# Kernel tuning notes

Measured on AMD Instinct MI355X. Metric: run time of the kernel, lower is better.

The kernel has to match this reference:

```python
import jax, jax.numpy as jnp
import numpy as np

N_QUBITS = 12
N_LAYERS = 2
DIM = 2 ** N_QUBITS  # 4096
BATCH = 1024


def _apply_gate(state, gate, qubit):
    """Apply a batched 2x2 gate to `qubit`. state: (b, 2^n) c64, gate: (b,2,2) c64.
    Mirrors torch _apply_single_qubit_gate: swap qubit axis to front, bmm, swap back."""
    b = state.shape[0]
    s = state.reshape((b,) + (2,) * N_QUBITS)
    ax = N_QUBITS - qubit  # qubit 0 is the last (least-significant) axis
    s = jnp.swapaxes(s, 1, ax)
    s = s.reshape(b, 2, DIM // 2)
    s = jnp.einsum('bij,bjk->bik', gate, s)
    s = s.reshape((b, 2) + (2,) * (N_QUBITS - 1))
    s = jnp.swapaxes(s, 1, ax)
    return s.reshape(b, DIM)


def _ry_gate(angle):
    """RY(theta) = [[cos(t/2), -sin(t/2)], [sin(t/2), cos(t/2)]]; angle: (b,)."""
    c = jnp.cos(angle / 2)
    s = jnp.sin(angle / 2)
    g = jnp.stack([jnp.stack([c, -s], axis=-1),
                   jnp.stack([s, c], axis=-1)], axis=-2)
    return g.astype(jnp.complex64)


def _apply_cnot(state, control, target):
    """CNOT: flip target amplitudes on the control=1 subspace."""
    b = state.shape[0]
    s = state.reshape((b,) + (2,) * N_QUBITS)
    ca = N_QUBITS - control
    ta = N_QUBITS - target
    s = jnp.moveaxis(s, (ca, ta), (1, 2))
    # control=0 slice unchanged; control=1 slice: swap target 0<->1 (flip)
    s = jnp.concatenate([s[:, :1], jnp.flip(s[:, 1:2], axis=2)], axis=1)
    s = jnp.moveaxis(s, (1, 2), (ca, ta))
    return s.reshape(b, DIM)


def _make_signs():
    # Pauli-Z expectation per qubit = sum_s probs[s] * (1 - 2*bit_q(s)); qubit 0 = LSB
    idx = np.arange(DIM)
    bits = (idx[:, None] >> np.arange(N_QUBITS)[None, :]) & 1
    return jnp.asarray(1.0 - 2.0 * bits, dtype=jnp.float32)  # (DIM, n_qubits)

SIGNS = _make_signs()


def setup_inputs() -> dict:
    key = jax.random.key(0)
    kx, kt = jax.random.split(key)
    x = jax.random.normal(kx, (BATCH, N_QUBITS), dtype=jnp.float32)
    thetas = 0.1 * jax.random.normal(kt, (N_LAYERS, N_QUBITS), dtype=jnp.float32)
    return {"x": x, "thetas": thetas}


def reference(x, thetas):
    b = x.shape[0]
    # |0>^n initial state
    state = jnp.zeros((b, DIM), dtype=jnp.complex64).at[:, 0].set(1.0)
    # angle encoding: RY(x_q) on each qubit
    for q in range(N_QUBITS):
        state = _apply_gate(state, _ry_gate(x[:, q]), q)
    # variational layers: RY(theta) per qubit, then cyclic CNOT ring
    for layer in range(N_LAYERS):
        for q in range(N_QUBITS):
            ang = jnp.broadcast_to(thetas[layer, q], (b,))
            state = _apply_gate(state, _ry_gate(ang), q)
        for q in range(N_QUBITS):
            state = _apply_cnot(state, q, (q + 1) % N_QUBITS)
    # Pauli-Z expectations on all qubits: (b, n_qubits)
    probs = jnp.abs(state) ** 2
    return probs @ SIGNS
```

## Files before the change

kernel.cpp:

```cpp
#include <hip/hip_runtime.h>

#define NQ    12
#define BATCH 1024

typedef float v2 __attribute__((ext_vector_type(2)));
typedef float v4 __attribute__((ext_vector_type(4)));

template<int P>
__device__ __forceinline__ void ryp_t(v2 A[16], float t) {
#pragma unroll
    for (int m = 0; m < 16; ++m) {
        if ((m & (1 << P)) == 0) {
            const int j = m | (1 << P);
            const v2 Ai = A[m], Aj = A[j];
            A[m] = Ai - t * Aj;
            A[j] = Aj + t * Ai;
        }
    }
}

__device__ __forceinline__ void ry0_t(v2 A[16], float t) {
    const v2 tv = v2{-t, t};
#pragma unroll
    for (int m = 0; m < 16; ++m) {
        const v2 sw = v2{A[m].y, A[m].x};
        A[m] = A[m] + tv * sw;
    }
}

__device__ __forceinline__ float rdlane(float v, int lane) {
    return __uint_as_float(__builtin_amdgcn_readlane(__float_as_uint(v), lane));
}

__global__ __launch_bounds__(128, 2)
void qc_kernel(const float* __restrict__ x, const float* __restrict__ th,
               float* __restrict__ out) {
    __shared__ __attribute__((aligned(16))) float buf1[2 * 32 * 68];
    __shared__ float obuf[12 * 2];

    const int b = blockIdx.x;
    const int w = threadIdx.x >> 6;
    const int l = threadIdx.x & 63;
    const float* xb = x + b * NQ;

    const int q_ = l & 31;
    float ang;
    if (l & 32) ang = (q_ < 12) ? 0.5f * th[NQ + q_] : 0.0f;
    else        { const int m_ = (q_ < 12) ? q_ : 11; ang = 0.5f * (xb[m_] + th[m_]); }
    float sv_, cv_;
    __sincosf(ang, &sv_, &cv_);
    const float tl = __fdividef(sv_, cv_);

    float pt = cv_;
    pt *= __shfl_xor(pt, 1, 64);
    pt *= __shfl_xor(pt, 2, 64);
    pt *= __shfl_xor(pt, 4, 64);
    pt *= __shfl_xor(pt, 8, 64);
    const float C = rdlane(pt, 32);

    float c_[NQ], s_[NQ], t1[NQ];
#pragma unroll
    for (int q = 0; q < NQ; ++q) {
        c_[q] = rdlane(cv_, q);
        s_[q] = rdlane(sv_, q);
        t1[q] = rdlane(tl, 32 + q);
    }

    const int l0=l&1, l1=(l>>1)&1, l2=(l>>2)&1, l3=(l>>3)&1, l4=(l>>4)&1, l5=(l>>5)&1;
    float GL = ((l1^l0) ? s_[6] : c_[6]) * ((l2^l1) ? s_[7] : c_[7]);
    GL *= ((l3^l2) ? s_[8] : c_[8]) * ((l4^l3) ? s_[9] : c_[9]);
    GL *= ((l5^l4) ? s_[10] : c_[10]) * ((w^l5) ? s_[11] : c_[11]);
    GL *= C;
    const float GL0 = GL * (l0 ? s_[5] : c_[5]);
    const float GL1 = GL * (l0 ? c_[5] : s_[5]);

    const float f0_0 = w ? s_[0] : c_[0], f0_1 = w ? c_[0] : s_[0];
    const float f1_0 = w ? s_[1] : c_[1], f1_1 = w ? c_[1] : s_[1];

    v2 A[16];
    A[0] = v2{f0_0 * f1_0, f0_1 * f1_1};
    A[1] = v2{f0_0 * f1_1, f0_1 * f1_0};
#pragma unroll
    for (int k = 2; k < 5; ++k) {
#pragma unroll
        for (int m = 0; m < (1 << (k - 1)); ++m) {
            const int bp = (m >> (k - 2)) & 1;
            A[m | (1 << (k - 1))] = A[m] * (bp ? c_[k] : s_[k]);
            A[m]                  = A[m] * (bp ? s_[k] : c_[k]);
        }
    }
#pragma unroll
    for (int m = 0; m < 16; ++m) A[m] *= (m & 8) ? GL1 : GL0;

    ry0_t(A, t1[0]);
    ryp_t<0>(A, t1[1]);
    ryp_t<1>(A, t1[2]);
    ryp_t<2>(A, t1[3]);
    ryp_t<3>(A, t1[4]);

    {
        float* wp = &buf1[w * 2176 + l];
#pragma unroll
        for (int m = 0; m < 16; ++m) {
            wp[(2*m)   * 68] = A[m].x;
            wp[(2*m+1) * 68] = A[m].y;
        }
    }
    __syncthreads();

    {
        const float s10 = (l & 32) ? t1[10] : -t1[10];
        const float s11 = w ? t1[11] : -t1[11];
        const int basec = (l & 31) * 68;
        const int ro = (l & 32);
        const int rf = ro ^ 32;
        const float* p00 = &buf1[ w      * 2176 + basec + ro];
        const float* p01 = &buf1[ w      * 2176 + basec + rf];
        const float* p10 = &buf1[(w ^ 1) * 2176 + basec + ro];
        const float* p11 = &buf1[(w ^ 1) * 2176 + basec + rf];
#pragma unroll
        for (int k = 0; k < 8; ++k) {
            const v4 a  = *reinterpret_cast<const v4*>(p00 + 4*k);
            const v4 bq = *reinterpret_cast<const v4*>(p01 + 4*k);
            const v4 cq = *reinterpret_cast<const v4*>(p10 + 4*k);
            const v4 dq = *reinterpret_cast<const v4*>(p11 + 4*k);
            const v4 u = a  + s10 * bq;
            const v4 v = cq + s10 * dq;
            const v4 r = u + s11 * v;
            A[2*k]   = v2{r.x, r.y};
            A[2*k+1] = v2{r.z, r.w};
        }
    }

    ry0_t(A, t1[5]);
    ryp_t<0>(A, t1[6]);
    ryp_t<1>(A, t1[7]);
    ryp_t<2>(A, t1[8]);
    ryp_t<3>(A, t1[9]);

#pragma unroll
    for (int m = 0; m < 16; ++m) A[m] *= A[m];

    float S = 0.f;
#pragma unroll
    for (int m = 0; m < 16; ++m) S += A[m].x + A[m].y;
    float d0[16];
#pragma unroll
    for (int m = 0; m < 16; ++m) d0[m] = A[m].x - A[m].y;
    float P1 = 0.f;
#pragma unroll
    for (int i = 0; i < 16; ++i) P1 += d0[i];
    float d1[8];
#pragma unroll
    for (int i = 0; i < 8; ++i) d1[i] = d0[2*i] - d0[2*i+1];
    float P3 = 0.f;
#pragma unroll
    for (int i = 0; i < 8; ++i) P3 += d1[i];
    float d2[4];
#pragma unroll
    for (int i = 0; i < 4; ++i) d2[i] = d1[2*i] - d1[2*i+1];
    const float P7  = d2[0] + d2[1] + d2[2] + d2[3];
    const float d3a = d2[0] - d2[1], d3b = d2[2] - d2[3];
    const float PF  = d3a + d3b;
    const float PV  = d3a - d3b;

    const int pl5 = __popc(l & 31) & 1;
    float y0 = pl5 ? -P1 : P1;
    float y1 = pl5 ? -P3 : P3;
    float y2 = pl5 ? -P7 : P7;
    float y3 = pl5 ? -PF : PF;
    y0 += __shfl_xor(y0, 1, 64); y1 += __shfl_xor(y1, 1, 64);
    y2 += __shfl_xor(y2, 1, 64); y3 += __shfl_xor(y3, 1, 64);
    y0 += __shfl_xor(y0, 2, 64); y1 += __shfl_xor(y1, 2, 64);
    y2 += __shfl_xor(y2, 2, 64); y3 += __shfl_xor(y3, 2, 64);
    const int g = l & 3;
    float y = (g == 0) ? y0 : (g == 1) ? y1 : (g == 2) ? y2 : y3;
    y += __shfl_xor(y,  4, 64);
    y += __shfl_xor(y,  8, 64);
    y += __shfl_xor(y, 16, 64);
    y += __shfl_xor(y, 32, 64);
    if (l < 4) obuf[(5 + l) * 2 + w] = y;

    float wS = S, wV = PV;
#pragma unroll
    for (int k = 0; k < 6; ++k) {
        float pS = __shfl_xor(wS, 1 << k, 64);
        wS = ((l >> k) & 1) ? (pS - wS) : (wS + pS);
        float pV = __shfl_xor(wV, 1 << k, 64);
        wV = ((l >> k) & 1) ? (pV - wV) : (wV + pV);
    }

    if (l == 3)  obuf[1*2 + w]  = wS;
    if (l == 7)  obuf[2*2 + w]  = wS;
    if (l == 15) obuf[3*2 + w]  = wS;
    if (l == 31) { obuf[4*2 + w] = wS; obuf[9*2 + w] = wV; }
    if (l == 62) obuf[0*2 + w]  = wV;
    if (l == 63) { obuf[10*2 + w] = wV; obuf[11*2 + w] = wV; }
    __syncthreads();

    if (threadIdx.x < NQ) {
        const int q = threadIdx.x;
        const float p0 = obuf[q*2 + 0], p1 = obuf[q*2 + 1];
        out[b * NQ + q] = (q == 0 || q == 11) ? (p0 - p1) : (p0 + p1);
    }
}

extern "C" void kernel_launch(void* const* d_in, const int* in_sizes, int n_in,
                              void* d_out, int out_size, void* d_ws, size_t ws_size,
                              hipStream_t stream) {
    const float* x  = (const float*)d_in[0];
    const float* th = (const float*)d_in[1];
    float* out = (float*)d_out;
    (void)in_sizes; (void)n_in; (void)out_size; (void)d_ws; (void)ws_size;

    qc_kernel<<<BATCH, 128, 0, stream>>>(x, th, out);
}
```

Before: 9.870 us.

## Pack four batch items per block and use DPP/swizzle for lane reductions

Each block now handles four batch elements with 512 threads instead of one element with 128, which cuts the grid to 256 blocks and gives each 128-thread group its own shared-memory slice. Cross-lane xor shuffles are replaced by DPP quad permutes and ds_swizzle, and the Walsh-style butterflies become FMA with a per-lane sign. The final parity reductions are also regrouped into vector adds. The bigger blocks use more shared memory each and share one __syncthreads, and with only 256 blocks on the device, occupancy and load balance may suffer.

```diff
diff --git a/kernel.cpp b/kernel.cpp
--- a/kernel.cpp
+++ b/kernel.cpp
@@ -32,16 +32,29 @@
     return __uint_as_float(__builtin_amdgcn_readlane(__float_as_uint(v), lane));
 }
 
-__global__ __launch_bounds__(128, 2)
+template<int CTRL>
+__device__ __forceinline__ float dppx(float v) {
+    return __int_as_float(__builtin_amdgcn_mov_dpp(__float_as_int(v), CTRL, 0xF, 0xF, true));
+}
+template<int PAT>
+__device__ __forceinline__ float swz(float v) {
+    return __int_as_float(__builtin_amdgcn_ds_swizzle(__float_as_int(v), PAT));
+}
+
+__global__ __launch_bounds__(512, 2)
 void qc_kernel(const float* __restrict__ x, const float* __restrict__ th,
                float* __restrict__ out) {
-    __shared__ __attribute__((aligned(16))) float buf1[2 * 32 * 68];
-    __shared__ float obuf[12 * 2];
-
-    const int b = blockIdx.x;
-    const int w = threadIdx.x >> 6;
-    const int l = threadIdx.x & 63;
+    __shared__ __attribute__((aligned(16))) float buf1[4 * 4352];
+    __shared__ float obuf[4 * 24];
+
+    const int tid = threadIdx.x;
+    const int p = tid >> 7;
+    const int w = (tid >> 6) & 1;
+    const int l = tid & 63;
+    const int b = blockIdx.x * 4 + p;
     const float* xb = x + b * NQ;
+    float* bufp  = &buf1[p * 4352];
+    float* obufp = &obuf[p * 24];
 
     const int q_ = l & 31;
     float ang;
@@ -52,10 +65,10 @@
     const float tl = __fdividef(sv_, cv_);
 
     float pt = cv_;
-    pt *= __shfl_xor(pt, 1, 64);
-    pt *= __shfl_xor(pt, 2, 64);
-    pt *= __shfl_xor(pt, 4, 64);
-    pt *= __shfl_xor(pt, 8, 64);
+    pt *= dppx<0xB1>(pt);
+    pt *= dppx<0x4E>(pt);
+    pt *= swz<0x101F>(pt);
+    pt *= swz<0x201F>(pt);
     const float C = rdlane(pt, 32);
 
     float c_[NQ], s_[NQ], t1[NQ];
@@ -99,7 +112,7 @@
     ryp_t<3>(A, t1[4]);
 
     {
-        float* wp = &buf1[w * 2176 + l];
+        float* wp = &bufp[w * 2176 + l];
 #pragma unroll
         for (int m = 0; m < 16; ++m) {
             wp[(2*m)   * 68] = A[m].x;
@@ -114,10 +127,10 @@
         const int basec = (l & 31) * 68;
         const int ro = (l & 32);
         const int rf = ro ^ 32;
-        const float* p00 = &buf1[ w      * 2176 + basec + ro];
-        const float* p01 = &buf1[ w      * 2176 + basec + rf];
-        const float* p10 = &buf1[(w ^ 1) * 2176 + basec + ro];
-        const float* p11 = &buf1[(w ^ 1) * 2176 + basec + rf];
+        const float* p00 = &bufp[ w      * 2176 + basec + ro];
+        const float* p01 = &bufp[ w      * 2176 + basec + rf];
+        const float* p10 = &bufp[(w ^ 1) * 2176 + basec + ro];
+        const float* p11 = &bufp[(w ^ 1) * 2176 + basec + rf];
 #pragma unroll
         for (int k = 0; k < 8; ++k) {
             const v4 a  = *reinterpret_cast<const v4*>(p00 + 4*k);
@@ -141,66 +154,68 @@
 #pragma unroll
     for (int m = 0; m < 16; ++m) A[m] *= A[m];
 
-    float S = 0.f;
-#pragma unroll
-    for (int m = 0; m < 16; ++m) S += A[m].x + A[m].y;
-    float d0[16];
-#pragma unroll
-    for (int m = 0; m < 16; ++m) d0[m] = A[m].x - A[m].y;
-    float P1 = 0.f;
-#pragma unroll
-    for (int i = 0; i < 16; ++i) P1 += d0[i];
-    float d1[8];
-#pragma unroll
-    for (int i = 0; i < 8; ++i) d1[i] = d0[2*i] - d0[2*i+1];
-    float P3 = 0.f;
-#pragma unroll
-    for (int i = 0; i < 8; ++i) P3 += d1[i];
-    float d2[4];
-#pragma unroll
-    for (int i = 0; i < 4; ++i) d2[i] = d1[2*i] - d1[2*i+1];
-    const float P7  = d2[0] + d2[1] + d2[2] + d2[3];
-    const float d3a = d2[0] - d2[1], d3b = d2[2] - d2[3];
-    const float PF  = d3a + d3b;
-    const float PV  = d3a - d3b;
+    v2 e[8], f[8];
+#pragma unroll
+    for (int i = 0; i < 8; ++i) { e[i] = A[2*i] + A[2*i+1]; f[i] = A[2*i] - A[2*i+1]; }
+    v2 se = ((e[0]+e[1]) + (e[2]+e[3])) + ((e[4]+e[5]) + (e[6]+e[7]));
+    v2 sf = ((f[0]+f[1]) + (f[2]+f[3])) + ((f[4]+f[5]) + (f[6]+f[7]));
+    v2 gq[4];
+#pragma unroll
+    for (int j = 0; j < 4; ++j) gq[j] = f[2*j] - f[2*j+1];
+    const v2 sg2 = (gq[0]+gq[1]) + (gq[2]+gq[3]);
+    const v2 h0 = gq[0] - gq[1], h1 = gq[2] - gq[3];
+    const v2 sh = h0 + h1;
+    const v2 iv = h0 - h1;
+    const float S  = se.x + se.y;
+    const float P1 = se.x - se.y;
+    const float P3 = sf.x - sf.y;
+    const float P7 = sg2.x - sg2.y;
+    const float PF = sh.x - sh.y;
+    const float PV = iv.x - iv.y;
 
     const int pl5 = __popc(l & 31) & 1;
     float y0 = pl5 ? -P1 : P1;
     float y1 = pl5 ? -P3 : P3;
     float y2 = pl5 ? -P7 : P7;
     float y3 = pl5 ? -PF : PF;
-    y0 += __shfl_xor(y0, 1, 64); y1 += __shfl_xor(y1, 1, 64);
-    y2 += __shfl_xor(y2, 1, 64); y3 += __shfl_xor(y3, 1, 64);
-    y0 += __shfl_xor(y0, 2, 64); y1 += __shfl_xor(y1, 2, 64);
-    y2 += __shfl_xor(y2, 2, 64); y3 += __shfl_xor(y3, 2, 64);
+    y0 += dppx<0xB1>(y0); y1 += dppx<0xB1>(y1);
+    y2 += dppx<0xB1>(y2); y3 += dppx<0xB1>(y3);
+    y0 += dppx<0x4E>(y0); y1 += dppx<0x4E>(y1);
+    y2 += dppx<0x4E>(y2); y3 += dppx<0x4E>(y3);
     const int g = l & 3;
     float y = (g == 0) ? y0 : (g == 1) ? y1 : (g == 2) ? y2 : y3;
-    y += __shfl_xor(y,  4, 64);
-    y += __shfl_xor(y,  8, 64);
-    y += __shfl_xor(y, 16, 64);
+    y += swz<0x101F>(y);
+    y += swz<0x201F>(y);
+    y += swz<0x401F>(y);
     y += __shfl_xor(y, 32, 64);
-    if (l < 4) obuf[(5 + l) * 2 + w] = y;
-
+    if (l < 4) obufp[(5 + l) * 2 + w] = y;
+
+    const float sg0 = (l & 1)  ? -1.f : 1.f;
+    const float sg1 = (l & 2)  ? -1.f : 1.f;
+    const float sg2s = (l & 4) ? -1.f : 1.f;
+    const float sg3 = (l & 8)  ? -1.f : 1.f;
+    const float sg4 = (l & 16) ? -1.f : 1.f;
+    const float sg5 = (l & 32) ? -1.f : 1.f;
     float wS = S, wV = PV;
-#pragma unroll
-    for (int k = 0; k < 6; ++k) {
-        float pS = __shfl_xor(wS, 1 << k, 64);
-        wS = ((l >> k) & 1) ? (pS - wS) : (wS + pS);
-        float pV = __shfl_xor(wV, 1 << k, 64);
-        wV = ((l >> k) & 1) ? (pV - wV) : (wV + pV);
-    }
-
-    if (l == 3)  obuf[1*2 + w]  = wS;
-    if (l == 7)  obuf[2*2 + w]  = wS;
-    if (l == 15) obuf[3*2 + w]  = wS;
-    if (l == 31) { obuf[4*2 + w] = wS; obuf[9*2 + w] = wV; }
-    if (l == 62) obuf[0*2 + w]  = wV;
-    if (l == 63) { obuf[10*2 + w] = wV; obuf[11*2 + w] = wV; }
+    { const float pS = dppx<0xB1>(wS),  pV = dppx<0xB1>(wV);  wS = __builtin_fmaf(sg0, wS, pS); wV = __builtin_fmaf(sg0, wV, pV); }
+    { const float pS = dppx<0x4E>(wS),  pV = dppx<0x4E>(wV);  wS = __builtin_fmaf(sg1, wS, pS); wV = __builtin_fmaf(sg1, wV, pV); }
+    { const float pS = swz<0x101F>(wS), pV = swz<0x101F>(wV); wS = __builtin_fmaf(sg2s, wS, pS); wV = __builtin_fmaf(sg2s, wV, pV); }
+    { const float pS = swz<0x201F>(wS), pV = swz<0x201F>(wV); wS = __builtin_fmaf(sg3, wS, pS); wV = __builtin_fmaf(sg3, wV, pV); }
+    { const float pS = swz<0x401F>(wS), pV = swz<0x401F>(wV); wS = __builtin_fmaf(sg4, wS, pS); wV = __builtin_fmaf(sg4, wV, pV); }
+    { const float pS = __shfl_xor(wS, 32, 64), pV = __shfl_xor(wV, 32, 64);
+      wS = __builtin_fmaf(sg5, wS, pS); wV = __builtin_fmaf(sg5, wV, pV); }
+
+    if (l == 3)  obufp[1*2 + w]  = wS;
+    if (l == 7)  obufp[2*2 + w]  = wS;
+    if (l == 15) obufp[3*2 + w]  = wS;
+    if (l == 31) { obufp[4*2 + w] = wS; obufp[9*2 + w] = wV; }
+    if (l == 62) obufp[0*2 + w]  = wV;
+    if (l == 63) { obufp[10*2 + w] = wV; obufp[11*2 + w] = wV; }
     __syncthreads();
 
-    if (threadIdx.x < NQ) {
-        const int q = threadIdx.x;
-        const float p0 = obuf[q*2 + 0], p1 = obuf[q*2 + 1];
+    if ((tid & 127) < NQ) {
+        const int q = tid & 127;
+        const float p0 = obufp[q*2 + 0], p1 = obufp[q*2 + 1];
         out[b * NQ + q] = (q == 0 || q == 11) ? (p0 - p1) : (p0 + p1);
     }
 }
@@ -213,5 +228,5 @@
     float* out = (float*)d_out;
     (void)in_sizes; (void)n_in; (void)out_size; (void)d_ws; (void)ws_size;
 
-    qc_kernel<<<BATCH, 128, 0, stream>>>(x, th, out);
-}
+    qc_kernel<<<BATCH / 4, 512, 0, stream>>>(x, th, out);
+}
```

After: 9.682 us. Within noise of the previous version (-1.9%).
